# Optimization experiments

Measured on AMD Instinct MI355X. Metric: run time of the kernel, lower is better.

The kernel has to match this reference:

```python
import jax, jax.numpy as jnp
import numpy as np

H = 64
W = 64
DIM = 256          # PatchExpand dim (= out_dim)
EPS = 1e-5         # nn.LayerNorm default eps


def setup_inputs() -> dict:
    key = jax.random.key(0)
    k1, k2 = jax.random.split(key)
    B = 16
    x1 = jax.random.normal(k1, (B, H * W, DIM), dtype=jnp.float32)
    # nn.Linear(dim, 2*dim, bias=False): weight shape [2*dim, dim], y = x @ W.T
    W_expand = jax.random.normal(k2, (2 * DIM, DIM), dtype=jnp.float32) * (1.0 / np.sqrt(DIM))
    ln_gamma = jnp.ones((DIM // 2,), dtype=jnp.float32)
    ln_beta = jnp.zeros((DIM // 2,), dtype=jnp.float32)
    return {"x1": x1, "W_expand": W_expand, "ln_gamma": ln_gamma, "ln_beta": ln_beta}


def _layernorm(x, gamma, beta):
    mu = jnp.mean(x, axis=-1, keepdims=True)
    var = jnp.mean(jnp.square(x - mu), axis=-1, keepdims=True)
    return (x - mu) * jax.lax.rsqrt(var + EPS) * gamma + beta


def reference(x1, W_expand, ln_gamma, ln_beta):
    # MyDecoderLayerDAEFormer.forward with x2=None -> PatchExpand(x1)
    B = x1.shape[0]
    c = DIM // 2
    # Linear expand: [B, H*W, dim] -> [B, H*W, 2*dim]
    x = jnp.einsum('bld,ed->ble', x1, W_expand)
    # b h w (p1 p2 c) -> b (h p1) (w p2) c, p1=p2=2
    x = x.reshape(B, H, W, 2, 2, c)
    x = x.transpose(0, 1, 3, 2, 4, 5).reshape(B, (2 * H) * (2 * W), c)
    return _layernorm(x, ln_gamma, ln_beta)
```

## Files before the change

kernel.cpp:

```cpp
#include <hip/hip_runtime.h>


typedef __attribute__((ext_vector_type(8))) short bf16x8;
typedef __attribute__((ext_vector_type(4))) float f32x4;

__device__ __forceinline__ unsigned short f2bf(float f) {
    unsigned u = __builtin_bit_cast(unsigned, f);
    u += 0x7fffu + ((u >> 16) & 1u);
    return (unsigned short)(u >> 16);
}

#define KPITCH 72

__global__ __launch_bounds__(512, 1)
void fused_expand_ln(const float* __restrict__ x1,
                     const float* __restrict__ Wg,
                     const float* __restrict__ gamma,
                     const float* __restrict__ beta,
                     float* __restrict__ out) {
    __shared__ unsigned short Alds[128 * KPITCH];
    __shared__ unsigned short Wlds[512 * KPITCH];

    const int tid  = threadIdx.x;
    const int l0   = blockIdx.x * 128;
    const int wid  = tid >> 6;
    const int lane = tid & 63;
    const int wm   = wid >> 2;
    const int wn   = wid & 3;
    const int g    = lane >> 4;
    const int c    = lane & 15;

    f32x4 acc[4][8];
#pragma unroll
    for (int i = 0; i < 4; ++i)
#pragma unroll
        for (int j = 0; j < 8; ++j) acc[i][j] = (f32x4){0.f, 0.f, 0.f, 0.f};

    const float4* x4 = reinterpret_cast<const float4*>(x1);
    const float4* w4 = reinterpret_cast<const float4*>(Wg);

    for (int kc = 0; kc < 4; ++kc) {
        const int kk4 = kc * 16;
#pragma unroll
        for (int j = 0; j < 4; ++j) {
            int fidx = tid + j * 512;
            int row = fidx >> 4, kq = fidx & 15;
            float4 v = x4[(size_t)(l0 + row) * 64 + kk4 + kq];
            ushort4 o = { f2bf(v.x), f2bf(v.y), f2bf(v.z), f2bf(v.w) };
            *reinterpret_cast<ushort4*>(&Alds[row * KPITCH + kq * 4]) = o;
        }
#pragma unroll
        for (int j = 0; j < 16; ++j) {
            int fidx = tid + j * 512;
            int row = fidx >> 4, kq = fidx & 15;
            float4 v = w4[(size_t)row * 64 + kk4 + kq];
            ushort4 o = { f2bf(v.x), f2bf(v.y), f2bf(v.z), f2bf(v.w) };
            *reinterpret_cast<ushort4*>(&Wlds[row * KPITCH + kq * 4]) = o;
        }
        __syncthreads();
#pragma unroll
        for (int ks = 0; ks < 2; ++ks) {
            const int koff = ks * 32 + g * 8;
            bf16x8 a[4], b[8];
#pragma unroll
            for (int mi = 0; mi < 4; ++mi)
                a[mi] = *reinterpret_cast<const bf16x8*>(
                    &Alds[(wm * 64 + mi * 16 + c) * KPITCH + koff]);
#pragma unroll
            for (int ni = 0; ni < 8; ++ni)
                b[ni] = *reinterpret_cast<const bf16x8*>(
                    &Wlds[(wn * 128 + ni * 16 + c) * KPITCH + koff]);
#pragma unroll
            for (int mi = 0; mi < 4; ++mi)
#pragma unroll
                for (int ni = 0; ni < 8; ++ni)
                    acc[mi][ni] = __builtin_amdgcn_mfma_f32_16x16x32_bf16(
                        a[mi], b[ni], acc[mi][ni], 0, 0, 0);
        }
        __syncthreads();
    }

    const int b  = l0 >> 12;
    const int h0 = (l0 & 4095) >> 6;
    const int p1 = wn >> 1, p2 = wn & 1;

    float gam[8], bet[8];
#pragma unroll
    for (int ni = 0; ni < 8; ++ni) {
        gam[ni] = gamma[ni * 16 + c];
        bet[ni] = beta[ni * 16 + c];
    }

    float* outp = out + (size_t)b * (16384 * 128);

#pragma unroll
    for (int mi = 0; mi < 4; ++mi) {
#pragma unroll
        for (int r = 0; r < 4; ++r) {
            float s = 0.f, q = 0.f;
#pragma unroll
            for (int ni = 0; ni < 8; ++ni) {
                float v = acc[mi][ni][r];
                s += v; q += v * v;
            }
#pragma unroll
            for (int m = 1; m < 16; m <<= 1) {
                s += __shfl_xor(s, m, 64);
                q += __shfl_xor(q, m, 64);
            }
            const float mean = s * (1.f / 128.f);
            const float var  = q * (1.f / 128.f) - mean * mean;
            const float rstd = rsqrtf(var + 1e-5f);

            const int i = wm * 64 + mi * 16 + g * 4 + r;
            const int h = h0 + (i >> 6);
            const int w = i & 63;
            const int orow = (2 * h + p1) * 128 + 2 * w + p2;
            float* orp = outp + (size_t)orow * 128;
#pragma unroll
            for (int ni = 0; ni < 8; ++ni) {
                float v = (acc[mi][ni][r] - mean) * rstd;
                orp[ni * 16 + c] = v * gam[ni] + bet[ni];
            }
        }
    }
}

extern "C" void kernel_launch(void* const* d_in, const int* in_sizes, int n_in,
                              void* d_out, int out_size, void* d_ws, size_t ws_size,
                              hipStream_t stream) {
    const float* x1   = (const float*)d_in[0];
    const float* Wg   = (const float*)d_in[1];
    const float* gam  = (const float*)d_in[2];
    const float* bet  = (const float*)d_in[3];
    float* out        = (float*)d_out;
    hipLaunchKernelGGL(fused_expand_ln, dim3(512), dim3(512), 0, stream,
                       x1, Wg, gam, bet, out);
}
```

Before: 240.7 us.

## Pre-convert weights to swizzled bf16 and halve row tile for occupancy

Adds a prep kernel that converts the weight matrix to bf16 once per call in an XOR-swizzled layout in workspace. The main kernel then loads it into LDS with direct global-to-LDS loads instead of converting the full weight in every block. The row tile drops from 128 to 64, which doubles the grid to 1024 blocks, and launch bounds allow 4 blocks per CU. LDS padding is replaced by an XOR swizzle to avoid bank conflicts. The cost is an extra kernel launch and a workspace dependency, with a fallback path when the workspace is too small.

After: 197.2 us. -18.0%, faster.

```diff
diff --git a/kernel.cpp b/kernel.cpp
--- a/kernel.cpp
+++ b/kernel.cpp
@@ -3,6 +3,7 @@
 
 typedef __attribute__((ext_vector_type(8))) short bf16x8;
 typedef __attribute__((ext_vector_type(4))) float f32x4;
+typedef __attribute__((ext_vector_type(8))) unsigned short u16x8;
 
 __device__ __forceinline__ unsigned short f2bf(float f) {
     unsigned u = __builtin_bit_cast(unsigned, f);
@@ -10,19 +11,37 @@
     return (unsigned short)(u >> 16);
 }
 
-#define KPITCH 72
+#define GLOAD_LDS16(g, l) __builtin_amdgcn_global_load_lds( \
+    (const __attribute__((address_space(1))) unsigned int*)(g), \
+    (__attribute__((address_space(3))) unsigned int*)(l), 16, 0, 0)
 
-__global__ __launch_bounds__(512, 1)
+__global__ void prep_w(const float* __restrict__ Wg, unsigned short* __restrict__ ws) {
+    int sg = blockIdx.x * 256 + threadIdx.x;
+    int row = sg >> 5;
+    int sl  = sg & 31;
+    int kc  = sl >> 3;
+    int s   = sl & 7;
+    const float4* w4 = reinterpret_cast<const float4*>(Wg + (size_t)row * 256 + kc * 64 + s * 8);
+    float4 v0 = w4[0], v1 = w4[1];
+    u16x8 o = { f2bf(v0.x), f2bf(v0.y), f2bf(v0.z), f2bf(v0.w),
+                f2bf(v1.x), f2bf(v1.y), f2bf(v1.z), f2bf(v1.w) };
+    char* dst = (char*)ws + kc * 65536 + row * 128 + ((s ^ (row & 7)) << 4);
+    *reinterpret_cast<u16x8*>(dst) = o;
+}
+
+template <bool WS>
+__global__ __launch_bounds__(512, 4)
 void fused_expand_ln(const float* __restrict__ x1,
                      const float* __restrict__ Wg,
+                     const unsigned short* __restrict__ wbf,
                      const float* __restrict__ gamma,
                      const float* __restrict__ beta,
                      float* __restrict__ out) {
-    __shared__ unsigned short Alds[128 * KPITCH];
-    __shared__ unsigned short Wlds[512 * KPITCH];
+    __shared__ unsigned short Alds[64 * 64];
+    __shared__ unsigned short Wlds[512 * 64];
 
     const int tid  = threadIdx.x;
-    const int l0   = blockIdx.x * 128;
+    const int l0   = blockIdx.x * 64;
     const int wid  = tid >> 6;
     const int lane = tid & 63;
     const int wm   = wid >> 2;
@@ -30,58 +49,68 @@
     const int g    = lane >> 4;
     const int c    = lane & 15;
 
-    f32x4 acc[4][8];
+    f32x4 acc[2][8];
 #pragma unroll
-    for (int i = 0; i < 4; ++i)
+    for (int i = 0; i < 2; ++i)
 #pragma unroll
         for (int j = 0; j < 8; ++j) acc[i][j] = (f32x4){0.f, 0.f, 0.f, 0.f};
 
-    const float4* x4 = reinterpret_cast<const float4*>(x1);
-    const float4* w4 = reinterpret_cast<const float4*>(Wg);
-
     for (int kc = 0; kc < 4; ++kc) {
-        const int kk4 = kc * 16;
+        {
+            int row = tid >> 3, s = tid & 7;
+            const float4* a4 = reinterpret_cast<const float4*>(
+                x1 + (size_t)(l0 + row) * 256 + kc * 64 + s * 8);
+            float4 v0 = a4[0], v1 = a4[1];
+            u16x8 o = { f2bf(v0.x), f2bf(v0.y), f2bf(v0.z), f2bf(v0.w),
+                        f2bf(v1.x), f2bf(v1.y), f2bf(v1.z), f2bf(v1.w) };
+            *reinterpret_cast<u16x8*>((char*)Alds + row * 128 + ((s ^ (row & 7)) << 4)) = o;
+        }
+        if (WS) {
 #pragma unroll
-        for (int j = 0; j < 4; ++j) {
-            int fidx = tid + j * 512;
-            int row = fidx >> 4, kq = fidx & 15;
-            float4 v = x4[(size_t)(l0 + row) * 64 + kk4 + kq];
-            ushort4 o = { f2bf(v.x), f2bf(v.y), f2bf(v.z), f2bf(v.w) };
-            *reinterpret_cast<ushort4*>(&Alds[row * KPITCH + kq * 4]) = o;
-        }
+            for (int it = 0; it < 8; ++it) {
+                const char* gp = (const char*)wbf + kc * 65536 + (tid + it * 512) * 16;
+                char* lp = (char*)Wlds + (tid + it * 512) * 16;
+                GLOAD_LDS16(gp, lp);
+            }
+        } else {
 #pragma unroll
-        for (int j = 0; j < 16; ++j) {
-            int fidx = tid + j * 512;
-            int row = fidx >> 4, kq = fidx & 15;
-            float4 v = w4[(size_t)row * 64 + kk4 + kq];
-            ushort4 o = { f2bf(v.x), f2bf(v.y), f2bf(v.z), f2bf(v.w) };
-            *reinterpret_cast<ushort4*>(&Wlds[row * KPITCH + kq * 4]) = o;
+            for (int j = 0; j < 8; ++j) {
+                int fidx = tid + j * 512;
+                int row = fidx >> 3, s = fidx & 7;
+                const float4* w4 = reinterpret_cast<const float4*>(
+                    Wg + (size_t)row * 256 + kc * 64 + s * 8);
+                float4 v0 = w4[0], v1 = w4[1];
+                u16x8 o = { f2bf(v0.x), f2bf(v0.y), f2bf(v0.z), f2bf(v0.w),
+                            f2bf(v1.x), f2bf(v1.y), f2bf(v1.z), f2bf(v1.w) };
+                *reinterpret_cast<u16x8*>((char*)Wlds + row * 128 + ((s ^ (row & 7)) << 4)) = o;
+            }
         }
         __syncthreads();
+
 #pragma unroll
         for (int ks = 0; ks < 2; ++ks) {
-            const int koff = ks * 32 + g * 8;
-            bf16x8 a[4], b[8];
+            const int sA = ks * 4 + g;
+            bf16x8 a[2];
 #pragma unroll
-            for (int mi = 0; mi < 4; ++mi)
+            for (int mi = 0; mi < 2; ++mi) {
+                int ra = wm * 32 + mi * 16 + c;
                 a[mi] = *reinterpret_cast<const bf16x8*>(
-                    &Alds[(wm * 64 + mi * 16 + c) * KPITCH + koff]);
+                    (const char*)Alds + ra * 128 + ((sA ^ (ra & 7)) << 4));
+            }
 #pragma unroll
-            for (int ni = 0; ni < 8; ++ni)
-                b[ni] = *reinterpret_cast<const bf16x8*>(
-                    &Wlds[(wn * 128 + ni * 16 + c) * KPITCH + koff]);
-#pragma unroll
-            for (int mi = 0; mi < 4; ++mi)
-#pragma unroll
-                for (int ni = 0; ni < 8; ++ni)
-                    acc[mi][ni] = __builtin_amdgcn_mfma_f32_16x16x32_bf16(
-                        a[mi], b[ni], acc[mi][ni], 0, 0, 0);
+            for (int ni = 0; ni < 8; ++ni) {
+                int rb = wn * 128 + ni * 16 + c;
+                bf16x8 b = *reinterpret_cast<const bf16x8*>(
+                    (const char*)Wlds + rb * 128 + ((sA ^ (rb & 7)) << 4));
+                acc[0][ni] = __builtin_amdgcn_mfma_f32_16x16x32_bf16(a[0], b, acc[0][ni], 0, 0, 0);
+                acc[1][ni] = __builtin_amdgcn_mfma_f32_16x16x32_bf16(a[1], b, acc[1][ni], 0, 0, 0);
+            }
         }
         __syncthreads();
     }
 
     const int b  = l0 >> 12;
-    const int h0 = (l0 & 4095) >> 6;
+    const int h  = (l0 & 4095) >> 6;
     const int p1 = wn >> 1, p2 = wn & 1;
 
     float gam[8], bet[8];
@@ -91,10 +120,10 @@
         bet[ni] = beta[ni * 16 + c];
     }
 
-    float* outp = out + (size_t)b * (16384 * 128);
+    float* outp = out + (size_t)b * (16384 * 128) + (size_t)(2 * h + p1) * (128 * 128);
 
 #pragma unroll
-    for (int mi = 0; mi < 4; ++mi) {
+    for (int mi = 0; mi < 2; ++mi) {
 #pragma unroll
         for (int r = 0; r < 4; ++r) {
             float s = 0.f, q = 0.f;
@@ -112,11 +141,8 @@
             const float var  = q * (1.f / 128.f) - mean * mean;
             const float rstd = rsqrtf(var + 1e-5f);
 
-            const int i = wm * 64 + mi * 16 + g * 4 + r;
-            const int h = h0 + (i >> 6);
-            const int w = i & 63;
-            const int orow = (2 * h + p1) * 128 + 2 * w + p2;
-            float* orp = outp + (size_t)orow * 128;
+            const int w = wm * 32 + mi * 16 + g * 4 + r;
+            float* orp = outp + (size_t)(2 * w + p2) * 128;
 #pragma unroll
             for (int ni = 0; ni < 8; ++ni) {
                 float v = (acc[mi][ni][r] - mean) * rstd;
@@ -129,11 +155,19 @@
 extern "C" void kernel_launch(void* const* d_in, const int* in_sizes, int n_in,
                               void* d_out, int out_size, void* d_ws, size_t ws_size,
                               hipStream_t stream) {
-    const float* x1   = (const float*)d_in[0];
-    const float* Wg   = (const float*)d_in[1];
-    const float* gam  = (const float*)d_in[2];
-    const float* bet  = (const float*)d_in[3];
-    float* out        = (float*)d_out;
-    hipLaunchKernelGGL(fused_expand_ln, dim3(512), dim3(512), 0, stream,
-                       x1, Wg, gam, bet, out);
+    const float* x1  = (const float*)d_in[0];
+    const float* Wg  = (const float*)d_in[1];
+    const float* gam = (const float*)d_in[2];
+    const float* bet = (const float*)d_in[3];
+    float* out       = (float*)d_out;
+
+    if (ws_size >= 262144) {
+        unsigned short* wbf = (unsigned short*)d_ws;
+        hipLaunchKernelGGL(prep_w, dim3(64), dim3(256), 0, stream, Wg, wbf);
+        hipLaunchKernelGGL((fused_expand_ln<true>), dim3(1024), dim3(512), 0, stream,
+                           x1, Wg, wbf, gam, bet, out);
+    } else {
+        hipLaunchKernelGGL((fused_expand_ln<false>), dim3(1024), dim3(512), 0, stream,
+                           x1, Wg, nullptr, gam, bet, out);
+    }
 }
```
